# Kernel optimization log

Hardware: AMD Instinct MI355X
Metric: run time of the kernel (lower is better)

Reference implementation:

```python
import jax, jax.numpy as jnp
import numpy as np

C = 768      # channel
H = 6        # height = 4 + 2*pre_step
W = 6        # width  = 4 + 2*pre_step
NB = 3       # n_block = H/2
SPLIT = 6    # = width
LS = 1536    # lstm_size = C * H / NB
NH = 4       # attention heads
DM = 512     # attention d_model
DK = DM // NH
B = 256


def setup_inputs() -> dict:
    key = jax.random.key(0)
    ks = jax.random.split(key, 20)
    s_l = 1.0 / np.sqrt(LS)
    s_a = 1.0 / np.sqrt(C)
    s_o = 1.0 / np.sqrt(DM)
    u = lambda k, shape, s: jax.random.uniform(k, shape, jnp.float32, -s, s)
    return {
        "x": jax.random.normal(ks[0], (B, H * W, C), jnp.float32),
        # 2-layer LSTM encoder (input=hidden=LS), torch gate order i,f,g,o
        "enc_Wih": u(ks[1], (2, 4 * LS, LS), s_l),
        "enc_Whh": u(ks[2], (2, 4 * LS, LS), s_l),
        "enc_bih": u(ks[3], (2, 4 * LS), s_l),
        "enc_bhh": u(ks[4], (2, 4 * LS), s_l),
        # 2-layer LSTM decoder
        "dec_Wih": u(ks[5], (2, 4 * LS, LS), s_l),
        "dec_Whh": u(ks[6], (2, 4 * LS, LS), s_l),
        "dec_bih": u(ks[7], (2, 4 * LS), s_l),
        "dec_bhh": u(ks[8], (2, 4 * LS), s_l),
        # multi-head attention: 768 -> 512 (4 heads x 128) -> 768
        "Wq": u(ks[9], (C, DM), s_a), "bq": u(ks[10], (DM,), s_a),
        "Wk": u(ks[11], (C, DM), s_a), "bk": u(ks[12], (DM,), s_a),
        "Wv": u(ks[13], (C, DM), s_a), "bv": u(ks[14], (DM,), s_a),
        "Wo": u(ks[15], (DM, C), s_o), "bo": u(ks[16], (C,), s_o),
        # LayerNorm over channel
        "ln_g": jnp.ones((C,), jnp.float32),
        "ln_b": jnp.zeros((C,), jnp.float32),
    }


def _cell(x, h, c, Wi, Wh, bi, bh):
    g = x @ Wi.T + bi + h @ Wh.T + bh
    i, f, gg, o = jnp.split(g, 4, axis=-1)
    c = jax.nn.sigmoid(f) * c + jax.nn.sigmoid(i) * jnp.tanh(gg)
    h = jax.nn.sigmoid(o) * jnp.tanh(c)
    return h, c


def _step2(st, xt, Wih, Whh, bih, bhh):
    # one timestep of a 2-layer LSTM
    h0, c0, h1, c1 = st
    h0, c0 = _cell(xt, h0, c0, Wih[0], Whh[0], bih[0], bhh[0])
    h1, c1 = _cell(h0, h1, c1, Wih[1], Whh[1], bih[1], bhh[1])
    return (h0, c0, h1, c1), h1


def _forward(x, enc_Wih, enc_Whh, enc_bih, enc_bhh,
             dec_Wih, dec_Whh, dec_bih, dec_bhh,
             Wq, bq, Wk, bk, Wv, bv, Wo, bo, ln_g, ln_b):
    Bx = x.shape[0]
    xb = x.reshape(Bx, NB, 2, W, C)
    # per block, each column j is a single-timestep feature concatenating the 2 rows
    # -> time-major sequence (SPLIT, NB*Bx, LS), blocks folded into the batch dim
    seq = jnp.transpose(xb, (3, 1, 0, 2, 4)).reshape(W, NB * Bx, LS)
    z = jnp.zeros((NB * Bx, LS), x.dtype)
    carry0 = (z, z, z, z)
    # encoder consumes columns in reversed order (j = split-1 .. 0)
    enc_st, enc_ys = jax.lax.scan(
        lambda s, xt: _step2(s, xt, enc_Wih, enc_Whh, enc_bih, enc_bhh),
        carry0, seq[::-1])
    en_out = enc_ys[-1]

    def dec_step(carry, _):
        st, inp = carry
        st, out = _step2(st, inp, dec_Wih, dec_Whh, dec_bih, dec_bhh)
        return (st, out), out
    _, dec_ys = jax.lax.scan(dec_step, (enc_st, en_out), None, length=SPLIT)

    # dec_ys: (SPLIT, NB*Bx, LS) -> xout_total: (NB, Bx, 2, SPLIT, C)
    xout = dec_ys.reshape(SPLIT, NB, Bx, 2, C).transpose(1, 2, 3, 0, 4)
    xt = xout.reshape(NB, Bx, 2 * SPLIT, C)

    # neighbor-block q/k, own-block v (NB=3): i=0 -> (q1,k2,v0); i=1 -> (q0,k2,v1); i=2 -> (q1,k0,v2)
    q = xt[jnp.array([1, 0, 1])]
    k = xt[jnp.array([2, 2, 0])]
    v = xt
    T = 2 * SPLIT
    Q = (q @ Wq + bq).reshape(NB, Bx, T, NH, DK)
    K = (k @ Wk + bk).reshape(NB, Bx, T, NH, DK)
    V = (v @ Wv + bv).reshape(NB, Bx, T, NH, DK)
    scores = jnp.einsum('nbqhd,nbkhd->nbhqk', Q, K) / np.float32(np.sqrt(DK))
    att = jax.nn.softmax(scores, axis=-1)
    o = jnp.einsum('nbhqk,nbkhd->nbqhd', att, V).reshape(NB, Bx, T, DM)
    o = o @ Wo + bo  # (NB, Bx, T, C)

    # concat blocks along height, layernorm over channel
    feat = o.reshape(NB, Bx, 2, W, C).transpose(1, 0, 2, 3, 4).reshape(Bx, H * W, C)
    mu = feat.mean(-1, keepdims=True)
    var = feat.var(-1, keepdims=True)
    feature = (feat - mu) / jnp.sqrt(var + 1e-5) * ln_g + ln_b
    out_decode = feature.reshape(Bx, H, W, C)[:, 1:5, 1:5, :]
    return feature, out_decode


def reference(x, enc_Wih, enc_Whh, enc_bih, enc_bhh,
              dec_Wih, dec_Whh, dec_bih, dec_bhh,
              Wq, bq, Wk, bk, Wv, bv, Wo, bo, ln_g, ln_b):
    return _forward(x, enc_Wih, enc_Whh, enc_bih, enc_bhh,
                    dec_Wih, dec_Whh, dec_bih, dec_bhh,
                    Wq, bq, Wk, bk, Wv, bv, Wo, bo, ln_g, ln_b)
```

## Files before the change

### kernel.cpp

```cpp
#include <hip/hip_runtime.h>


typedef unsigned short u16;
typedef unsigned int   u32;
typedef __bf16 bf16x8 __attribute__((ext_vector_type(8)));
typedef short  short8 __attribute__((ext_vector_type(8)));
typedef float  f32x4  __attribute__((ext_vector_type(4)));

__device__ __forceinline__ u16 f2bf(float f) {
  u32 u = __float_as_uint(f);
  u32 r = u + 0x7FFFu + ((u >> 16) & 1u);
  return (u16)(r >> 16);
}

__device__ __forceinline__ f32x4 mfma16(short8 a, short8 b, f32x4 c) {
  return __builtin_amdgcn_mfma_f32_16x16x32_bf16(
      __builtin_bit_cast(bf16x8, a), __builtin_bit_cast(bf16x8, b), c, 0, 0, 0);
}

__device__ __forceinline__ void gload16(const u16* g, u16* l) {
  __builtin_amdgcn_global_load_lds(
      (const __attribute__((address_space(1))) u32*)g,
      (__attribute__((address_space(3))) u32*)l, 16, 0, 0);
}

__global__ __launch_bounds__(512) void lstm_cell(
    const u16* __restrict__ X, const u16* __restrict__ H,
    const u16* __restrict__ Wih, const u16* __restrict__ Whh,
    const float* __restrict__ bi, const float* __restrict__ bh,
    float* __restrict__ c, u16* __restrict__ hout, u16* __restrict__ h2)
{
  __shared__ __align__(16) u16 smem[36864];
  const int tid  = threadIdx.x;
  const int wid   = ((blockIdx.x & 7) << 5) + (blockIdx.x >> 3);
  const int strip = wid >> 3;
  const int bm    = wid & 7;
  const int strip48 = strip * 48;
  const int lane = tid & 63, wave = tid >> 6;
  const int gq = wave >> 1, mh = wave & 1;
  const int r16  = lane & 15, kg = lane >> 4;
  const int srow = lane >> 2, sslot = lane & 3;

  f32x4 acc[3][3];
#pragma unroll
  for (int mi = 0; mi < 3; ++mi)
#pragma unroll
    for (int ni = 0; ni < 3; ++ni) acc[mi][ni] = (f32x4)0.0f;

  auto stage = [&](int s) {
    const int slot = s & 3;
    const u16* Aptr = (s < 48) ? X : H;
    const u16* W    = (s < 48) ? Wih : Whh;
    const int k0 = ((s < 48) ? s : (s - 48)) << 5;
    if (wave < 2) {
#pragma unroll
      for (int cc = 0; cc < 3; ++cc) {
        const int call = wave * 3 + cc;
        const int row  = call * 16 + srow;
        const int slog = sslot ^ ((row >> 1) & 3);
        gload16(Aptr + (size_t)(bm * 96 + row) * 1536 + k0 + slog * 8,
                smem + slot * 3072 + call * 512);
      }
    } else {
#pragma unroll
      for (int cc = 0; cc < 2; ++cc) {
        const int cb   = (wave - 2) * 2 + cc;
        const int rb   = cb * 16 + srow;
        const int g    = cb / 3;
        const int hh   = rb - g * 48;
        const int slog = sslot ^ ((rb >> 1) & 3);
        gload16(W + ((size_t)g * 1536 + strip48 + hh) * 1536 + k0 + slog * 8,
                smem + 12288 + slot * 6144 + cb * 512);
      }
    }
  };

  auto computeFrom = [&](int s) {
    const int slot = s & 3;
    const u16* baseA = smem + slot * 3072;
    const u16* baseB = smem + 12288 + slot * 6144;
    short8 af[3];
#pragma unroll
    for (int mi = 0; mi < 3; ++mi) {
      const int row = mh * 48 + mi * 16 + r16;
      af[mi] = *(const short8*)(baseA + row * 32 + ((kg ^ ((row >> 1) & 3)) << 3));
    }
    short8 bfr[3];
#pragma unroll
    for (int ni = 0; ni < 3; ++ni) {
      const int rb = gq * 48 + ni * 16 + r16;
      bfr[ni] = *(const short8*)(baseB + rb * 32 + ((kg ^ ((rb >> 1) & 3)) << 3));
    }
#pragma unroll
    for (int mi = 0; mi < 3; ++mi)
#pragma unroll
      for (int ni = 0; ni < 3; ++ni)
        acc[mi][ni] = mfma16(af[mi], bfr[ni], acc[mi][ni]);
  };

  stage(0); stage(1); stage(2); stage(3);

  for (int i = 0; i < 92; ++i) {
    if (wave < 2) asm volatile("s_waitcnt vmcnt(9)" ::: "memory");
    else          asm volatile("s_waitcnt vmcnt(6)" ::: "memory");
    __builtin_amdgcn_sched_barrier(0);
    __builtin_amdgcn_s_barrier();
    computeFrom(i);
    __builtin_amdgcn_s_barrier();
    __builtin_amdgcn_sched_barrier(0);
    stage(i + 4);
  }
  if (wave < 2) asm volatile("s_waitcnt vmcnt(9)" ::: "memory");
  else          asm volatile("s_waitcnt vmcnt(6)" ::: "memory");
  __builtin_amdgcn_sched_barrier(0);
  __builtin_amdgcn_s_barrier();
  computeFrom(92);
  if (wave < 2) asm volatile("s_waitcnt vmcnt(6)" ::: "memory");
  else          asm volatile("s_waitcnt vmcnt(4)" ::: "memory");
  __builtin_amdgcn_sched_barrier(0);
  __builtin_amdgcn_s_barrier();
  computeFrom(93);
  if (wave < 2) asm volatile("s_waitcnt vmcnt(3)" ::: "memory");
  else          asm volatile("s_waitcnt vmcnt(2)" ::: "memory");
  __builtin_amdgcn_sched_barrier(0);
  __builtin_amdgcn_s_barrier();
  computeFrom(94);
  asm volatile("s_waitcnt vmcnt(0)" ::: "memory");
  __builtin_amdgcn_sched_barrier(0);
  __builtin_amdgcn_s_barrier();
  computeFrom(95);
  __builtin_amdgcn_s_barrier();

  float* sG = (float*)smem;
#pragma unroll
  for (int mi = 0; mi < 3; ++mi)
#pragma unroll
    for (int ni = 0; ni < 3; ++ni)
#pragma unroll
      for (int j = 0; j < 4; ++j) {
        const int row = mh * 48 + mi * 16 + kg * 4 + j;
        const int h   = ni * 16 + r16;
        sG[gq * 4608 + row * 48 + h] = acc[mi][ni][j];
      }
  __syncthreads();

#pragma unroll
  for (int k = 0; k < 9; ++k) {
    const int e   = tid + k * 512;
    const int row = e / 48;
    const int h   = e - row * 48;
    const int hg  = strip48 + h;
    const float ig = sG[e]            + bi[hg]        + bh[hg];
    const float fg = sG[4608 + e]     + bi[1536 + hg] + bh[1536 + hg];
    const float gz = sG[9216 + e]     + bi[3072 + hg] + bh[3072 + hg];
    const float og = sG[13824 + e]    + bi[4608 + hg] + bh[4608 + hg];
    const float si = 1.0f / (1.0f + expf(-ig));
    const float sf = 1.0f / (1.0f + expf(-fg));
    const float so = 1.0f / (1.0f + expf(-og));
    const size_t cij = (size_t)(bm * 96 + row) * 1536 + hg;
    const float cnew = sf * c[cij] + si * tanhf(gz);
    c[cij] = cnew;
    const u16 hv = f2bf(so * tanhf(cnew));
    hout[cij] = hv;
    if (h2) h2[cij] = hv;
  }
}

template <int OUT_BF16, int HAS_BIAS>
__global__ __launch_bounds__(256, 2) void gemm_bt(
    const u16* __restrict__ A1, const u16* __restrict__ B1, int K1,
    const float* __restrict__ bias, void* __restrict__ Cout, int N)
{
  __shared__ __align__(16) u16 smem[16384];
  const int tid  = threadIdx.x;
  const int bn   = blockIdx.x * 128;
  const int bm   = blockIdx.y * 128;
  const int lane = tid & 63, wave = tid >> 6;
  const int wm   = (wave >> 1) * 64, wn = (wave & 1) * 64;
  const int r16  = lane & 15, kg = lane >> 4;
  const int srow = lane >> 2, sslot = lane & 3;

  f32x4 acc[4][4];
#pragma unroll
  for (int i = 0; i < 4; ++i)
#pragma unroll
    for (int j = 0; j < 4; ++j) acc[i][j] = (f32x4)0.0f;

  const int nt = K1 >> 5;
  auto stage = [&](int i, int buf) {
    const int k0 = i << 5;
#pragma unroll
    for (int cc2 = 0; cc2 < 2; ++cc2) {
      const int call = wave * 2 + cc2;
      const int row  = call * 16 + srow;
      const int slog = sslot ^ ((row >> 1) & 3);
      gload16(A1 + (size_t)(bm + row) * K1 + k0 + slog * 8, smem + buf * 4096 + call * 512);
      gload16(B1 + (size_t)(bn + row) * K1 + k0 + slog * 8, smem + 8192 + buf * 4096 + call * 512);
    }
  };

  stage(0, 0);
  __syncthreads();
  int cur = 0;
  for (int i = 0; i < nt; ++i) {
    if (i + 1 < nt) stage(i + 1, cur ^ 1);
    const u16* baseA = smem + cur * 4096;
    const u16* baseB = smem + 8192 + cur * 4096;
    short8 af[4], bfr[4];
#pragma unroll
    for (int mi = 0; mi < 4; ++mi) {
      const int row = wm + mi * 16 + r16;
      af[mi] = *(const short8*)(baseA + row * 32 + ((kg ^ ((row >> 1) & 3)) << 3));
    }
#pragma unroll
    for (int ni = 0; ni < 4; ++ni) {
      const int row = wn + ni * 16 + r16;
      bfr[ni] = *(const short8*)(baseB + row * 32 + ((kg ^ ((row >> 1) & 3)) << 3));
    }
#pragma unroll
    for (int mi = 0; mi < 4; ++mi)
#pragma unroll
      for (int ni = 0; ni < 4; ++ni)
        acc[mi][ni] = mfma16(af[mi], bfr[ni], acc[mi][ni]);
    __syncthreads();
    cur ^= 1;
  }

  const size_t Ns = (size_t)N;
#pragma unroll
  for (int ni = 0; ni < 4; ++ni) {
    const int col = bn + wn + ni * 16 + r16;
    const float bvv = HAS_BIAS ? bias[col] : 0.0f;
#pragma unroll
    for (int mi = 0; mi < 4; ++mi) {
      const int row0 = bm + wm + mi * 16 + kg * 4;
      f32x4 v = acc[mi][ni];
#pragma unroll
      for (int j = 0; j < 4; ++j) {
        const float val = v[j] + bvv;
        const size_t idx = (size_t)(row0 + j) * Ns + col;
        if (OUT_BF16) ((u16*)Cout)[idx] = f2bf(val);
        else          ((float*)Cout)[idx] = val;
      }
    }
  }
}

__global__ __launch_bounds__(256) void attn_kernel(const u16* __restrict__ P, u16* __restrict__ O)
{
  __shared__ __align__(16) u16 sQ[12 * 520];
  __shared__ __align__(16) u16 sK[12 * 520];
  __shared__ __align__(16) u16 sVT[512 * 24];
  __shared__ __align__(16) u16 sS[4 * 16 * 16];
  const int tid = threadIdx.x;
  const int nb = blockIdx.x >> 8;
  const int b  = blockIdx.x & 255;
  const int qb = (nb == 1) ? 0 : 1;
  const int kb = (nb == 2) ? 0 : 2;
  const size_t rq = ((size_t)qb * 256 + b) * 12;
  const size_t rk = ((size_t)kb * 256 + b) * 12;
  const size_t rv = ((size_t)nb * 256 + b) * 12;

  for (int e4 = tid; e4 < 1536; e4 += 256) {
    const int t  = e4 >> 7;
    const int cc = (e4 & 127) * 4;
    uint2 qv = *(const uint2*)(P + (rq + t) * 1536 + cc);
    *(uint2*)(sQ + t * 520 + cc) = qv;
    uint2 kv = *(const uint2*)(P + (rk + t) * 1536 + 512 + cc);
    *(uint2*)(sK + t * 520 + cc) = kv;
    uint2 vv = *(const uint2*)(P + (rv + t) * 1536 + 1024 + cc);
    sVT[(cc + 0) * 24 + t] = (u16)(vv.x & 0xffff);
    sVT[(cc + 1) * 24 + t] = (u16)(vv.x >> 16);
    sVT[(cc + 2) * 24 + t] = (u16)(vv.y & 0xffff);
    sVT[(cc + 3) * 24 + t] = (u16)(vv.y >> 16);
  }
  for (int i = tid; i < 2048; i += 256) sVT[(i >> 2) * 24 + 12 + (i & 3)] = 0;
  __syncthreads();

  const int lane = tid & 63, h = tid >> 6;
  const int r16 = lane & 15, kg = lane >> 4;
  const int hcol = h * 128;

  f32x4 sc = (f32x4)0.0f;
#pragma unroll
  for (int ks = 0; ks < 4; ++ks) {
    short8 aq  = (r16 < 12) ? *(const short8*)(sQ + r16 * 520 + hcol + ks * 32 + kg * 8) : (short8)0;
    short8 bk2 = (r16 < 12) ? *(const short8*)(sK + r16 * 520 + hcol + ks * 32 + kg * 8) : (short8)0;
    sc = mfma16(aq, bk2, sc);
  }
  const float scale = 0.08838834764831845f;
#pragma unroll
  for (int j = 0; j < 4; ++j) {
    float v = (r16 < 12) ? sc[j] * scale : -1e30f;
    float m = v;
#pragma unroll
    for (int d = 1; d < 16; d <<= 1) m = fmaxf(m, __shfl_xor(m, d));
    float e = expf(v - m);
    float s = e;
#pragma unroll
    for (int d = 1; d < 16; d <<= 1) s += __shfl_xor(s, d);
    sS[h * 256 + (kg * 4 + j) * 16 + r16] = f2bf(e / s);
  }
  __syncthreads();
  short8 av = (kg < 2) ? *(const short8*)(sS + h * 256 + r16 * 16 + kg * 8) : (short8)0;
#pragma unroll
  for (int dt = 0; dt < 8; ++dt) {
    short8 bv2 = (kg < 2) ? *(const short8*)(sVT + (hcol + dt * 16 + r16) * 24 + kg * 8) : (short8)0;
    f32x4 ov = mfma16(av, bv2, (f32x4)0.0f);
    if (kg < 3) {
#pragma unroll
      for (int j = 0; j < 4; ++j) {
        const int q = kg * 4 + j;
        O[(rv + q) * 512 + hcol + dt * 16 + r16] = f2bf(ov[j]);
      }
    }
  }
}

__global__ __launch_bounds__(256) void layernorm_kernel(
    const float* __restrict__ feat, const float* __restrict__ gam,
    const float* __restrict__ bet, float* __restrict__ out)
{
  const int row = blockIdx.x;
  const int b = row / 36, hidx = row - b * 36;
  const int nb = hidx / 12, t = hidx - nb * 12;
  const float* src = feat + ((size_t)nb * 3072 + b * 12 + t) * 768;
  const int tid = threadIdx.x;
  float v0 = src[tid], v1 = src[tid + 256], v2 = src[tid + 512];
  float s = v0 + v1 + v2, sq = v0 * v0 + v1 * v1 + v2 * v2;
#pragma unroll
  for (int d = 1; d < 64; d <<= 1) { s += __shfl_xor(s, d); sq += __shfl_xor(sq, d); }
  __shared__ float ps[4], pq[4];
  if ((tid & 63) == 0) { ps[tid >> 6] = s; pq[tid >> 6] = sq; }
  __syncthreads();
  s  = ps[0] + ps[1] + ps[2] + ps[3];
  sq = pq[0] + pq[1] + pq[2] + pq[3];
  const float mean = s * (1.0f / 768.0f);
  const float var  = sq * (1.0f / 768.0f) - mean * mean;
  const float rstd = rsqrtf(var + 1e-5f);
  float* dst = out + (size_t)row * 768;
  const int hh = hidx / 6, wp = hidx - hh * 6;
  float* dst2 = nullptr;
  if (hh >= 1 && hh < 5 && wp >= 1 && wp < 5)
    dst2 = out + 7077888 + ((size_t)b * 16 + (hh - 1) * 4 + (wp - 1)) * 768;
#pragma unroll
  for (int i = 0; i < 3; ++i) {
    const int cix = tid + i * 256;
    const float vv = (i == 0) ? v0 : (i == 1 ? v1 : v2);
    const float o = (vv - mean) * rstd * gam[cix] + bet[cix];
    dst[cix] = o;
    if (dst2) dst2[cix] = o;
  }
}

__global__ __launch_bounds__(256) void cast_bf16_kernel(const float* __restrict__ src,
                                                        u16* __restrict__ dst, int n4)
{
  const int i = blockIdx.x * 256 + threadIdx.x;
  if (i >= n4) return;
  float4 v = ((const float4*)src)[i];
  uint2 pk;
  pk.x = (u32)f2bf(v.x) | ((u32)f2bf(v.y) << 16);
  pk.y = (u32)f2bf(v.z) | ((u32)f2bf(v.w) << 16);
  ((uint2*)dst)[i] = pk;
}

__global__ __launch_bounds__(256) void pack_qkvT(const float* __restrict__ Wq,
    const float* __restrict__ Wk, const float* __restrict__ Wv, u16* __restrict__ dst)
{
  const int idx = blockIdx.x * 256 + threadIdx.x;
  if (idx >= 1536 * 768) return;
  const int d = idx / 768, c = idx - d * 768;
  float v;
  if (d < 512)       v = Wq[(size_t)c * 512 + d];
  else if (d < 1024) v = Wk[(size_t)c * 512 + d - 512];
  else               v = Wv[(size_t)c * 512 + d - 1024];
  dst[idx] = f2bf(v);
}

__global__ __launch_bounds__(256) void pack_bias(const float* __restrict__ bq,
    const float* __restrict__ bk, const float* __restrict__ bv, float* __restrict__ dst)
{
  const int i = blockIdx.x * 256 + threadIdx.x;
  if (i < 512)       dst[i] = bq[i];
  else if (i < 1024) dst[i] = bk[i - 512];
  else if (i < 1536) dst[i] = bv[i - 1024];
}

__global__ __launch_bounds__(256) void pack_WoT(const float* __restrict__ Wo, u16* __restrict__ dst)
{
  const int idx = blockIdx.x * 256 + threadIdx.x;
  if (idx >= 768 * 512) return;
  const int n = idx / 512, k = idx - n * 512;
  dst[idx] = f2bf(Wo[(size_t)k * 768 + n]);
}

__global__ __launch_bounds__(256) void build_Xe(const float* __restrict__ x, u16* __restrict__ Xe)
{
  const int i4 = blockIdx.x * 256 + threadIdx.x;
  if (i4 >= 1769472) return;
  const int e = i4 * 4;
  const int c = e % 768;
  const int r2 = (e / 768) & 1;
  const int r = (e / 1536) % 768;
  const int s = e / 1179648;
  const int nb = r >> 8, bb = r & 255;
  const int w = 5 - s;
  const float* src = x + ((size_t)bb * 36 + (nb * 2 + r2) * 6 + w) * 768 + c;
  float4 v = *(const float4*)src;
  uint2 pk;
  pk.x = (u32)f2bf(v.x) | ((u32)f2bf(v.y) << 16);
  pk.y = (u32)f2bf(v.z) | ((u32)f2bf(v.w) << 16);
  ((uint2*)Xe)[i4] = pk;
}

__global__ __launch_bounds__(256) void build_xt(const u16* __restrict__ decys, u16* __restrict__ xt)
{
  const int i4 = blockIdx.x * 256 + threadIdx.x;
  if (i4 >= 1769472) return;
  const int e = i4 * 4;
  const int c = e % 768;
  const int t = (e / 768) % 12;
  const int b = (e / 9216) % 256;
  const int nb = e / 2359296;
  const int r2 = t / 6, s = t - r2 * 6;
  const u16* src = decys + ((size_t)s * 768 + nb * 256 + b) * 1536 + r2 * 768 + c;
  ((uint2*)xt)[i4] = *(const uint2*)src;
}

extern "C" void kernel_launch(void* const* d_in, const int* in_sizes, int n_in,
                              void* d_out, int out_size, void* d_ws, size_t ws_size,
                              hipStream_t stream)
{
  const float* x    = (const float*)d_in[0];
  const float* eWih = (const float*)d_in[1];
  const float* eWhh = (const float*)d_in[2];
  const float* ebih = (const float*)d_in[3];
  const float* ebhh = (const float*)d_in[4];
  const float* dWih = (const float*)d_in[5];
  const float* dWhh = (const float*)d_in[6];
  const float* dbih = (const float*)d_in[7];
  const float* dbhh = (const float*)d_in[8];
  const float* Wq = (const float*)d_in[9];
  const float* bq = (const float*)d_in[10];
  const float* Wk = (const float*)d_in[11];
  const float* bk = (const float*)d_in[12];
  const float* Wv = (const float*)d_in[13];
  const float* bv = (const float*)d_in[14];
  const float* Wo = (const float*)d_in[15];
  const float* bo = (const float*)d_in[16];
  const float* lng = (const float*)d_in[17];
  const float* lnb = (const float*)d_in[18];

  char* ws = (char*)d_ws;
  const size_t WBYTES = 37748736;
  u16* Weih = (u16*)(ws);
  u16* Wehh = (u16*)(ws + WBYTES);
  u16* Wdih = (u16*)(ws + 2 * WBYTES);
  u16* Wdhh = (u16*)(ws + 3 * WBYTES);
  u16*   xtb   = (u16*)(ws);
  u16*   Pqkv  = (u16*)(ws + 14155776);
  u16*   Obuf  = (u16*)(ws + 14155776 + 28311552);
  float* feato = (float*)(ws + 14155776 + 28311552 + 9437184);
  size_t off = 4 * WBYTES;
  auto take = [&](size_t bytes) -> char* {
    char* p = ws + off;
    off = (off + bytes + 255) & ~(size_t)255;
    return p;
  };
  u16* Wqkv  = (u16*)take((size_t)1536 * 768 * 2);
  float* bqkv = (float*)take(1536 * 4);
  u16* WoT   = (u16*)take((size_t)768 * 512 * 2);
  u16* Xe    = (u16*)take((size_t)6 * 768 * 1536 * 2);
  u16* h0a   = (u16*)take((size_t)768 * 1536 * 2);
  u16* h0b   = (u16*)take((size_t)768 * 1536 * 2);
  u16* h1a   = (u16*)take((size_t)768 * 1536 * 2);
  u16* h1b   = (u16*)take((size_t)768 * 1536 * 2);
  float* c0  = (float*)take((size_t)768 * 1536 * 4);
  float* c1  = (float*)take((size_t)768 * 1536 * 4);
  u16* decys = (u16*)take((size_t)6 * 768 * 1536 * 2);
  if (off > ws_size) return;

  const size_t WL = (size_t)6144 * 1536;
  const dim3 blk(256);
  const dim3 blkCell(512);

  cast_bf16_kernel<<<18432, blk, 0, stream>>>(eWih, Weih, 4718592);
  cast_bf16_kernel<<<18432, blk, 0, stream>>>(eWhh, Wehh, 4718592);
  cast_bf16_kernel<<<18432, blk, 0, stream>>>(dWih, Wdih, 4718592);
  cast_bf16_kernel<<<18432, blk, 0, stream>>>(dWhh, Wdhh, 4718592);
  pack_qkvT<<<4608, blk, 0, stream>>>(Wq, Wk, Wv, Wqkv);
  pack_bias<<<6, blk, 0, stream>>>(bq, bk, bv, bqkv);
  pack_WoT<<<1536, blk, 0, stream>>>(Wo, WoT);
  build_Xe<<<6912, blk, 0, stream>>>(x, Xe);

  hipMemsetAsync(h0a, 0, (size_t)768 * 1536 * 2, stream);
  hipMemsetAsync(h1a, 0, (size_t)768 * 1536 * 2, stream);
  hipMemsetAsync(c0, 0, (size_t)768 * 1536 * 4, stream);
  hipMemsetAsync(c1, 0, (size_t)768 * 1536 * 4, stream);

  u16* h0[2] = {h0a, h0b};
  u16* h1[2] = {h1a, h1b};
  int p = 0;
  for (int s = 0; s < 6; ++s) {
    lstm_cell<<<256, blkCell, 0, stream>>>(Xe + (size_t)s * 768 * 1536, h0[p],
                                           Weih, Wehh, ebih, ebhh, c0, h0[p ^ 1], nullptr);
    lstm_cell<<<256, blkCell, 0, stream>>>(h0[p ^ 1], h1[p],
                                           Weih + WL, Wehh + WL, ebih + 6144, ebhh + 6144,
                                           c1, h1[p ^ 1], nullptr);
    p ^= 1;
  }
  for (int t = 0; t < 6; ++t) {
    lstm_cell<<<256, blkCell, 0, stream>>>(h1[p], h0[p],
                                           Wdih, Wdhh, dbih, dbhh, c0, h0[p ^ 1], nullptr);
    lstm_cell<<<256, blkCell, 0, stream>>>(h0[p ^ 1], h1[p],
                                           Wdih + WL, Wdhh + WL, dbih + 6144, dbhh + 6144,
                                           c1, h1[p ^ 1], decys + (size_t)t * 768 * 1536);
    p ^= 1;
  }
  build_xt<<<6912, blk, 0, stream>>>(decys, xtb);
  gemm_bt<1, 1><<<dim3(12, 72), blk, 0, stream>>>(xtb, Wqkv, 768, bqkv, Pqkv, 1536);
  attn_kernel<<<768, blk, 0, stream>>>(Pqkv, Obuf);
  gemm_bt<0, 1><<<dim3(6, 72), blk, 0, stream>>>(Obuf, WoT, 512, bo, feato, 768);
  layernorm_kernel<<<9216, blk, 0, stream>>>(feato, lng, lnb, (float*)d_out);
}
```

Before: 1.350 ms.

## Halve LSTM cell tile width to launch 512 smaller 256-thread blocks

The LSTM cell kernel now gives each block a 96x96 gate tile (24 hidden units x 4 gates) instead of 96x192, using 256 threads and 48 KB LDS. The grid grows from 256 to 512 blocks, with launch bounds allowing two blocks per CU. The aim is to fill more of the machine on this small per-step GEMM and to let two blocks overlap their load and compute phases. In exchange, the A (activation) tile is loaded twice as often across blocks, and the per-block MFMA work per loaded byte drops.

```diff
diff --git a/kernel.cpp b/kernel.cpp
--- a/kernel.cpp
+++ b/kernel.cpp
@@ -24,20 +24,20 @@
       (__attribute__((address_space(3))) u32*)l, 16, 0, 0);
 }
 
-__global__ __launch_bounds__(512) void lstm_cell(
+__global__ __launch_bounds__(256, 2) void lstm_cell(
     const u16* __restrict__ X, const u16* __restrict__ H,
     const u16* __restrict__ Wih, const u16* __restrict__ Whh,
     const float* __restrict__ bi, const float* __restrict__ bh,
     float* __restrict__ c, u16* __restrict__ hout, u16* __restrict__ h2)
 {
-  __shared__ __align__(16) u16 smem[36864];
+  __shared__ __align__(16) u16 smem[24576];
   const int tid  = threadIdx.x;
-  const int wid   = ((blockIdx.x & 7) << 5) + (blockIdx.x >> 3);
+  const int wid   = ((blockIdx.x & 7) << 6) + (blockIdx.x >> 3);
   const int strip = wid >> 3;
   const int bm    = wid & 7;
-  const int strip48 = strip * 48;
+  const int strip24 = strip * 24;
   const int lane = tid & 63, wave = tid >> 6;
-  const int gq = wave >> 1, mh = wave & 1;
+  const int mh = wave & 1, gh = wave >> 1;
   const int r16  = lane & 15, kg = lane >> 4;
   const int srow = lane >> 2, sslot = lane & 3;
 
@@ -52,25 +52,22 @@
     const u16* Aptr = (s < 48) ? X : H;
     const u16* W    = (s < 48) ? Wih : Whh;
     const int k0 = ((s < 48) ? s : (s - 48)) << 5;
-    if (wave < 2) {
-#pragma unroll
-      for (int cc = 0; cc < 3; ++cc) {
-        const int call = wave * 3 + cc;
+#pragma unroll
+    for (int cc = 0; cc < 3; ++cc) {
+      const int call = wave * 3 + cc;
+      if (call < 6) {
         const int row  = call * 16 + srow;
         const int slog = sslot ^ ((row >> 1) & 3);
         gload16(Aptr + (size_t)(bm * 96 + row) * 1536 + k0 + slog * 8,
                 smem + slot * 3072 + call * 512);
-      }
-    } else {
-#pragma unroll
-      for (int cc = 0; cc < 2; ++cc) {
-        const int cb   = (wave - 2) * 2 + cc;
+      } else {
+        const int cb   = call - 6;
         const int rb   = cb * 16 + srow;
-        const int g    = cb / 3;
-        const int hh   = rb - g * 48;
+        const int g    = rb / 24;
+        const int hh   = rb - g * 24;
         const int slog = sslot ^ ((rb >> 1) & 3);
-        gload16(W + ((size_t)g * 1536 + strip48 + hh) * 1536 + k0 + slog * 8,
-                smem + 12288 + slot * 6144 + cb * 512);
+        gload16(W + ((size_t)g * 1536 + strip24 + hh) * 1536 + k0 + slog * 8,
+                smem + 12288 + slot * 3072 + cb * 512);
       }
     }
   };
@@ -78,7 +75,7 @@
   auto computeFrom = [&](int s) {
     const int slot = s & 3;
     const u16* baseA = smem + slot * 3072;
-    const u16* baseB = smem + 12288 + slot * 6144;
+    const u16* baseB = smem + 12288 + slot * 3072;
     short8 af[3];
 #pragma unroll
     for (int mi = 0; mi < 3; ++mi) {
@@ -88,7 +85,7 @@
     short8 bfr[3];
 #pragma unroll
     for (int ni = 0; ni < 3; ++ni) {
-      const int rb = gq * 48 + ni * 16 + r16;
+      const int rb = gh * 48 + ni * 16 + r16;
       bfr[ni] = *(const short8*)(baseB + rb * 32 + ((kg ^ ((rb >> 1) & 3)) << 3));
     }
 #pragma unroll
@@ -101,8 +98,7 @@
   stage(0); stage(1); stage(2); stage(3);
 
   for (int i = 0; i < 92; ++i) {
-    if (wave < 2) asm volatile("s_waitcnt vmcnt(9)" ::: "memory");
-    else          asm volatile("s_waitcnt vmcnt(6)" ::: "memory");
+    asm volatile("s_waitcnt vmcnt(9)" ::: "memory");
     __builtin_amdgcn_sched_barrier(0);
     __builtin_amdgcn_s_barrier();
     computeFrom(i);
@@ -110,18 +106,15 @@
     __builtin_amdgcn_sched_barrier(0);
     stage(i + 4);
   }
-  if (wave < 2) asm volatile("s_waitcnt vmcnt(9)" ::: "memory");
-  else          asm volatile("s_waitcnt vmcnt(6)" ::: "memory");
+  asm volatile("s_waitcnt vmcnt(9)" ::: "memory");
   __builtin_amdgcn_sched_barrier(0);
   __builtin_amdgcn_s_barrier();
   computeFrom(92);
-  if (wave < 2) asm volatile("s_waitcnt vmcnt(6)" ::: "memory");
-  else          asm volatile("s_waitcnt vmcnt(4)" ::: "memory");
+  asm volatile("s_waitcnt vmcnt(6)" ::: "memory");
   __builtin_amdgcn_sched_barrier(0);
   __builtin_amdgcn_s_barrier();
   computeFrom(93);
-  if (wave < 2) asm volatile("s_waitcnt vmcnt(3)" ::: "memory");
-  else          asm volatile("s_waitcnt vmcnt(2)" ::: "memory");
+  asm volatile("s_waitcnt vmcnt(3)" ::: "memory");
   __builtin_amdgcn_sched_barrier(0);
   __builtin_amdgcn_s_barrier();
   computeFrom(94);
@@ -129,7 +122,7 @@
   __builtin_amdgcn_sched_barrier(0);
   __builtin_amdgcn_s_barrier();
   computeFrom(95);
-  __builtin_amdgcn_s_barrier();
+  __syncthreads();
 
   float* sG = (float*)smem;
 #pragma unroll
@@ -138,22 +131,24 @@
     for (int ni = 0; ni < 3; ++ni)
 #pragma unroll
       for (int j = 0; j < 4; ++j) {
-        const int row = mh * 48 + mi * 16 + kg * 4 + j;
-        const int h   = ni * 16 + r16;
-        sG[gq * 4608 + row * 48 + h] = acc[mi][ni][j];
+        const int row  = mh * 48 + mi * 16 + kg * 4 + j;
+        const int gcol = gh * 48 + ni * 16 + r16;
+        const int g    = gcol / 24;
+        const int h    = gcol - g * 24;
+        sG[g * 2304 + row * 24 + h] = acc[mi][ni][j];
       }
   __syncthreads();
 
 #pragma unroll
   for (int k = 0; k < 9; ++k) {
-    const int e   = tid + k * 512;
-    const int row = e / 48;
-    const int h   = e - row * 48;
-    const int hg  = strip48 + h;
-    const float ig = sG[e]            + bi[hg]        + bh[hg];
-    const float fg = sG[4608 + e]     + bi[1536 + hg] + bh[1536 + hg];
-    const float gz = sG[9216 + e]     + bi[3072 + hg] + bh[3072 + hg];
-    const float og = sG[13824 + e]    + bi[4608 + hg] + bh[4608 + hg];
+    const int e   = tid + k * 256;
+    const int row = e / 24;
+    const int h   = e - row * 24;
+    const int hg  = strip24 + h;
+    const float ig = sG[e]           + bi[hg]        + bh[hg];
+    const float fg = sG[2304 + e]    + bi[1536 + hg] + bh[1536 + hg];
+    const float gz = sG[4608 + e]    + bi[3072 + hg] + bh[3072 + hg];
+    const float og = sG[6912 + e]    + bi[4608 + hg] + bh[4608 + hg];
     const float si = 1.0f / (1.0f + expf(-ig));
     const float sf = 1.0f / (1.0f + expf(-fg));
     const float so = 1.0f / (1.0f + expf(-og));
@@ -483,7 +478,6 @@
 
   const size_t WL = (size_t)6144 * 1536;
   const dim3 blk(256);
-  const dim3 blkCell(512);
 
   cast_bf16_kernel<<<18432, blk, 0, stream>>>(eWih, Weih, 4718592);
   cast_bf16_kernel<<<18432, blk, 0, stream>>>(eWhh, Wehh, 4718592);
@@ -503,19 +497,19 @@
   u16* h1[2] = {h1a, h1b};
   int p = 0;
   for (int s = 0; s < 6; ++s) {
-    lstm_cell<<<256, blkCell, 0, stream>>>(Xe + (size_t)s * 768 * 1536, h0[p],
-                                           Weih, Wehh, ebih, ebhh, c0, h0[p ^ 1], nullptr);
-    lstm_cell<<<256, blkCell, 0, stream>>>(h0[p ^ 1], h1[p],
-                                           Weih + WL, Wehh + WL, ebih + 6144, ebhh + 6144,
-                                           c1, h1[p ^ 1], nullptr);
+    lstm_cell<<<512, blk, 0, stream>>>(Xe + (size_t)s * 768 * 1536, h0[p],
+                                       Weih, Wehh, ebih, ebhh, c0, h0[p ^ 1], nullptr);
+    lstm_cell<<<512, blk, 0, stream>>>(h0[p ^ 1], h1[p],
+                                       Weih + WL, Wehh + WL, ebih + 6144, ebhh + 6144,
+                                       c1, h1[p ^ 1], nullptr);
     p ^= 1;
   }
   for (int t = 0; t < 6; ++t) {
-    lstm_cell<<<256, blkCell, 0, stream>>>(h1[p], h0[p],
-                                           Wdih, Wdhh, dbih, dbhh, c0, h0[p ^ 1], nullptr);
-    lstm_cell<<<256, blkCell, 0, stream>>>(h0[p ^ 1], h1[p],
-                                           Wdih + WL, Wdhh + WL, dbih + 6144, dbhh + 6144,
-                                           c1, h1[p ^ 1], decys + (size_t)t * 768 * 1536);
+    lstm_cell<<<512, blk, 0, stream>>>(h1[p], h0[p],
+                                       Wdih, Wdhh, dbih, dbhh, c0, h0[p ^ 1], nullptr);
+    lstm_cell<<<512, blk, 0, stream>>>(h0[p ^ 1], h1[p],
+                                       Wdih + WL, Wdhh + WL, dbih + 6144, dbhh + 6144,
+                                       c1, h1[p ^ 1], decys + (size_t)t * 768 * 1536);
     p ^= 1;
   }
   build_xt<<<6912, blk, 0, stream>>>(decys, xtb);
```

Measured after the change: 1.410 ms. 4.4% more time.
